# Optimization experiments

Measured on AMD Instinct MI355X. Metric: run time of the kernel, lower is better.

Reference implementation:

```python
import jax, jax.numpy as jnp
import numpy as np

# cfg dims: B batch, LQ max_que_len, O max_opt_count, LO max_opt_len,
# S max_sent_para, W max_words_sent, D word_emb
B, LQ, O, LO, S, W, D = 64, 64, 8, 32, 64, 32, 512
NEG_BIG = -9.0e15  # torch masked_fill constant for empty sentences


def setup_inputs() -> dict:
    key = jax.random.key(0)
    k1, k2, k3 = jax.random.split(key, 3)
    que_feat = jax.random.normal(k1, (B, LQ, D), dtype=jnp.float32)
    opt_feat = jax.random.normal(k2, (B, O, LO, D), dtype=jnp.float32)
    csf = jax.random.normal(k3, (B, S, W, D), dtype=jnp.float32)
    csf_mask = jnp.zeros((B, S, W), dtype=bool)   # True = padding word
    opt_sum = jnp.zeros((B, O), dtype=bool)       # True = empty option
    return dict(que_feat=que_feat, opt_feat=opt_feat, csf=csf,
                csf_mask=csf_mask, opt_sum=opt_sum)


def reference(que_feat, opt_feat, csf, csf_mask, opt_sum):
    b, s, w, d = csf.shape
    o = opt_feat.shape[1]

    # per-sentence valid length; empty sentences get a huge-magnitude divisor
    csf_len = jnp.sum(~csf_mask, axis=-1)                      # [B,S]
    csf_len = jnp.where(csf_len == 0, NEG_BIG,
                        csf_len.astype(jnp.float32))

    # question -> context sentence score: sum over query words and sentence
    # words of dot products (original: matmul + two sums, fused here)
    att_q2c = jnp.einsum('bqd,bswd->bs', que_feat, csf)        # [B,S]
    ix_q2c = jnp.argmax(att_q2c / csf_len, axis=-1)            # [B]

    # gather best sentence per batch item, broadcast over options
    que_csf = jnp.take_along_axis(
        csf, ix_q2c[:, None, None, None], axis=1)[:, 0]        # [B,W,D]
    que_csf = jnp.broadcast_to(que_csf[:, None], (b, o, w, d))
    que_csf = jnp.where(opt_sum[:, :, None, None], 0.0, que_csf)

    # option -> context sentence score
    att_o2c = jnp.einsum('bold,bswd->bos', opt_feat, csf)      # [B,O,S]
    ix_o2c = jnp.argmax(att_o2c / csf_len[:, None, :], axis=-1)  # [B,O]

    # faithful to original get_opt2csf: indexes csf[0] for EVERY batch item
    opt_csf = csf[0][ix_o2c]                                   # [B,O,W,D]
    opt_csf = jnp.where(opt_sum[:, :, None, None], 0.0, opt_csf)

    # make_mask: positions whose feature vector is all-zero
    que_csf_mask = jnp.sum(jnp.abs(que_csf), axis=-1) == 0     # [B,O,W]
    opt_csf_mask = jnp.sum(jnp.abs(opt_csf), axis=-1) == 0     # [B,O,W]
    return que_csf, que_csf_mask, opt_csf, opt_csf_mask
```

## Files before the change

kernel.cpp:

```cpp
#include <hip/hip_runtime.h>
#include <hip/hip_cooperative_groups.h>
#include <stddef.h>

namespace cg = cooperative_groups;

#define B  64
#define LQ 64
#define O  8
#define LO 32
#define S  64
#define W  32
#define D  512

#define NEG_BIG (-9.0e15f)

#define QUE_CSF_SZ  (B*O*W*D)
#define MASK_SZ     (B*O*W)
#define OFF_QMASK   (QUE_CSF_SZ)
#define OFF_OPT     (QUE_CSF_SZ + MASK_SZ)
#define OFF_OMASK   (QUE_CSF_SZ + MASK_SZ + QUE_CSF_SZ)

#define WS_QSUMH 0
#define WS_OSUM  (B*2*D)
#define WS_SC    (B*2*D + B*O*D)

#define NBLK 2368

using f4 = __attribute__((ext_vector_type(4))) float;

__device__ inline float dot4(f4 a, f4 b) {
  return a.x * b.x + a.y * b.y + a.z * b.z + a.w * b.w;
}

#define RED(v)                \
  do {                        \
    v += __shfl_xor(v, 32);   \
    v += __shfl_xor(v, 16);   \
    v += __shfl_xor(v, 8);    \
    v += __shfl_xor(v, 4);    \
    v += __shfl_xor(v, 2);    \
    v += __shfl_xor(v, 1);    \
  } while (0)

__device__ inline f4 stream32(const f4* __restrict__ p, int t) {
  f4 acc = {0.f, 0.f, 0.f, 0.f};
  #pragma unroll 8
  for (int r = 0; r < 32; ++r) acc += p[(size_t)r * 128 + t];
  return acc;
}

__device__ inline void dots9(const float* __restrict__ ws, f4 acc, int b,
                             int wv, int lane, float part[2][9]) {
  const f4* qh = (const f4*)(ws + WS_QSUMH) + (size_t)b * 256;
  const int t = wv * 64 + lane;
  f4 qs = qh[t] + qh[128 + t];
  float pq = dot4(acc, qs);
  float po[O];
  #pragma unroll
  for (int o = 0; o < O; ++o)
    po[o] = dot4(acc, ((const f4*)(ws + WS_OSUM))[((size_t)(b * O + o)) * 128 + t]);
  RED(pq);
  #pragma unroll
  for (int o = 0; o < O; ++o) RED(po[o]);
  if (lane == 0) {
    part[wv][0] = pq;
    #pragma unroll
    for (int o = 0; o < O; ++o) part[wv][1 + o] = po[o];
  }
}

__global__ __launch_bounds__(128, 5) void k_fused(
    const float* __restrict__ que, const float* __restrict__ opt,
    const float* __restrict__ csf, const unsigned char* __restrict__ csf_mask,
    float* __restrict__ ws) {
  const int blk = blockIdx.x;
  const int t = threadIdx.x;
  const int wv = t >> 6;
  const int lane = t & 63;
  const int g1 = blk + NBLK;
  const bool j1csf = (g1 < 4096);

  f4 acc0 = stream32((const f4*)csf + (size_t)blk * 4096, t);
  f4 acc1;
  if (j1csf) {
    acc1 = stream32((const f4*)csf + (size_t)g1 * 4096, t);
  } else if (g1 < 4224) {
    const int idx = g1 - 4096;
    const int b = idx >> 1, h = idx & 1;
    acc1 = stream32((const f4*)que + ((size_t)b * LQ + h * 32) * 128, t);
    ((f4*)(ws + WS_QSUMH))[(size_t)idx * 128 + t] = acc1;
  } else {
    const int bo = g1 - 4224;
    acc1 = stream32((const f4*)opt + (size_t)bo * LO * 128, t);
    ((f4*)(ws + WS_OSUM))[(size_t)bo * 128 + t] = acc1;
  }

  __threadfence();
  cg::this_grid().sync();

  __shared__ float part[2][2][9];
  dots9(ws, acc0, blk >> 6, wv, lane, part[0]);
  if (j1csf) dots9(ws, acc1, g1 >> 6, wv, lane, part[1]);

  float len;
  {
    const int bs = (wv == 0) ? blk : g1;
    int pad = 0;
    if (lane < W && (wv == 0 || j1csf))
      pad = (csf_mask[(size_t)bs * W + lane] != 0) ? 1 : 0;
    const unsigned long long bal = __ballot(pad);
    const int valid = W - (int)__popcll(bal);
    len = (valid == 0) ? NEG_BIG : (float)valid;
  }
  __syncthreads();

  if (t < 9) {
    const int b0 = blk >> 6, s0 = blk & 63;
    ws[WS_SC + ((size_t)t * B + b0) * S + s0] =
        (part[0][0][t] + part[0][1][t]) / len;
  }
  if (j1csf && t >= 64 && t < 73) {
    const int q = t - 64;
    const int b1 = g1 >> 6, s1 = g1 & 63;
    ws[WS_SC + ((size_t)q * B + b1) * S + s1] =
        (part[1][0][q] + part[1][1][q]) / len;
  }
}

template <int ROWS>
__device__ inline void rowsum4(const f4* __restrict__ src, f4* __restrict__ dst,
                               int t) {
  const int quarter = t >> 7;
  const int col = t & 127;
  const f4* p = src + (size_t)(quarter * (ROWS / 4)) * 128 + col;
  f4 acc = {0.f, 0.f, 0.f, 0.f};
  #pragma unroll
  for (int r = 0; r < ROWS / 4; ++r) acc += p[(size_t)r * 128];
  __shared__ f4 tmp[3][128];
  if (quarter) tmp[quarter - 1][col] = acc;
  __syncthreads();
  if (quarter == 0) dst[col] = acc + tmp[0][col] + tmp[1][col] + tmp[2][col];
}

__global__ __launch_bounds__(512) void k_qosum(
    const float* __restrict__ que, const float* __restrict__ opt,
    float* __restrict__ ws) {
  const int blk = blockIdx.x;
  const int t = threadIdx.x;
  if (blk < B) {
    rowsum4<LQ>((const f4*)que + (size_t)blk * LQ * 128,
                (f4*)(ws + WS_QSUMH) + (size_t)blk * 256, t);
    if (t < 128) {
      f4 z = {0.f, 0.f, 0.f, 0.f};
      ((f4*)(ws + WS_QSUMH))[(size_t)blk * 256 + 128 + t] = z;
    }
  } else {
    const int bo = blk - B;
    rowsum4<LO>((const f4*)opt + (size_t)bo * LO * 128,
                (f4*)(ws + WS_OSUM) + (size_t)bo * 128, t);
  }
}

__global__ __launch_bounds__(128) void k_score(
    const float* __restrict__ csf, const unsigned char* __restrict__ csf_mask,
    float* __restrict__ ws) {
  const int bs = blockIdx.x;
  const int b = bs >> 6;
  const int s = bs & 63;
  const int t = threadIdx.x;
  const int wv = t >> 6;
  const int lane = t & 63;

  f4 acc = stream32((const f4*)csf + (size_t)bs * 4096, t);

  __shared__ float part[2][9];
  dots9(ws, acc, b, wv, lane, part);

  int pad = 0;
  if (lane < W) pad = (csf_mask[(size_t)bs * W + lane] != 0) ? 1 : 0;
  const unsigned long long bal = __ballot(pad);
  const int valid = W - (int)__popcll(bal);
  const float len = (valid == 0) ? NEG_BIG : (float)valid;

  __syncthreads();
  if (t < 9)
    ws[WS_SC + ((size_t)t * B + b) * S + s] = (part[0][t] + part[1][t]) / len;
}

__global__ __launch_bounds__(128) void k_gather(
    const float* __restrict__ csf, const unsigned char* __restrict__ opt_sum,
    const float* __restrict__ ws, float* __restrict__ out) {
  const int bow = blockIdx.x;
  const int w = bow & 31;
  const int bo = bow >> 5;
  const int b = bo >> 3;
  const int o = bo & 7;
  const int t = threadIdx.x;
  const int wv = t >> 6;
  const int lane = t & 63;

  __shared__ int sh_ix[2];
  {
    const int q = (wv == 0) ? 0 : (1 + o);
    float v = ws[WS_SC + ((size_t)q * B + b) * S + lane];
    int idx = lane;
    for (int off = 32; off; off >>= 1) {
      float ov = __shfl_xor(v, off);
      int oi = __shfl_xor(idx, off);
      if (ov > v || (ov == v && oi < idx)) { v = ov; idx = oi; }
    }
    if (lane == 0) sh_ix[wv] = idx;
  }
  __syncthreads();

  const bool zero = (opt_sum[bo] != 0);
  f4 vq = {0.f, 0.f, 0.f, 0.f};
  f4 vo = {0.f, 0.f, 0.f, 0.f};
  if (!zero) {
    const int iq = sh_ix[0];
    const int io = sh_ix[1];
    vq = ((const f4*)csf)[(((size_t)b * S + iq) * W + w) * 128 + t];
    vo = ((const f4*)csf)[((size_t)io * W + w) * 128 + t];
  }
  __builtin_nontemporal_store(vq, (f4*)(out + (size_t)bow * D) + t);
  __builtin_nontemporal_store(vo, (f4*)(out + OFF_OPT + (size_t)bow * D) + t);

  float aq = fabsf(vq.x) + fabsf(vq.y) + fabsf(vq.z) + fabsf(vq.w);
  float ao = fabsf(vo.x) + fabsf(vo.y) + fabsf(vo.z) + fabsf(vo.w);
  for (int off = 32; off; off >>= 1) {
    aq += __shfl_xor(aq, off);
    ao += __shfl_xor(ao, off);
  }

  __shared__ float sq[2], so[2];
  if (lane == 0) { sq[wv] = aq; so[wv] = ao; }
  __syncthreads();
  if (t == 0) {
    out[OFF_QMASK + bow] = ((sq[0] + sq[1]) == 0.f) ? 1.f : 0.f;
    out[OFF_OMASK + bow] = ((so[0] + so[1]) == 0.f) ? 1.f : 0.f;
  }
}

extern "C" void kernel_launch(void* const* d_in, const int* in_sizes, int n_in,
                              void* d_out, int out_size, void* d_ws, size_t ws_size,
                              hipStream_t stream) {
  const float* que = (const float*)d_in[0];
  const float* opt = (const float*)d_in[1];
  const float* csf = (const float*)d_in[2];
  const unsigned char* csf_mask = (const unsigned char*)d_in[3];
  const unsigned char* opt_sum = (const unsigned char*)d_in[4];
  float* out = (float*)d_out;
  float* ws = (float*)d_ws;

  int coop = 0;
  {
    int dev = 0;
    hipDeviceProp_t prop{};
    int mb = 0;
    if (hipGetDevice(&dev) == hipSuccess &&
        hipGetDeviceProperties(&prop, dev) == hipSuccess &&
        hipOccupancyMaxActiveBlocksPerMultiprocessor(&mb, k_fused, 128, 0) ==
            hipSuccess) {
      if (prop.cooperativeLaunch &&
          (long)mb * prop.multiProcessorCount >= NBLK)
        coop = 1;
    }
  }

  if (coop) {
    void* args[] = {(void*)&que, (void*)&opt, (void*)&csf, (void*)&csf_mask,
                    (void*)&ws};
    if (hipLaunchCooperativeKernel(k_fused, dim3(NBLK), dim3(128), args, 0,
                                   stream) != hipSuccess)
      coop = 0;
  }
  if (!coop) {
    k_qosum<<<B + B * O, 512, 0, stream>>>(que, opt, ws);
    k_score<<<B * S, 128, 0, stream>>>(csf, csf_mask, ws);
  }

  k_gather<<<B * O * W, 128, 0, stream>>>(csf, opt_sum, ws, out);
}
```

Before: 70.63 us.

## Fuse gather phase into cooperative kernel behind a second grid sync

Moves the argmax plus gather/mask stage into the cooperative fused kernel after an extra grid barrier. Each wave handles one output row in a grid-stride loop, which removes the separate k_gather launch. The two streaming reductions are also interleaved in one loop so their loads can overlap. In exchange it adds a second grid-wide sync, and the gather runs at 128-thread occupancy with the argmax recomputed per row.

New measurement: 70.59 us. About the same (-0.1%).

```diff
diff --git a/kernel.cpp b/kernel.cpp
--- a/kernel.cpp
+++ b/kernel.cpp
@@ -42,12 +42,14 @@
     v += __shfl_xor(v, 1);    \
   } while (0)
 
-__device__ inline f4 stream32(const f4* __restrict__ p, int t) {
-  f4 acc = {0.f, 0.f, 0.f, 0.f};
-  #pragma unroll 8
-  for (int r = 0; r < 32; ++r) acc += p[(size_t)r * 128 + t];
-  return acc;
-}
+#define ARGMAX(v, idx)                                         \
+  do {                                                         \
+    for (int off_ = 32; off_; off_ >>= 1) {                    \
+      float ov_ = __shfl_xor(v, off_);                         \
+      int oi_ = __shfl_xor(idx, off_);                         \
+      if (ov_ > v || (ov_ == v && oi_ < idx)) { v = ov_; idx = oi_; } \
+    }                                                          \
+  } while (0)
 
 __device__ inline void dots9(const float* __restrict__ ws, f4 acc, int b,
                              int wv, int lane, float part[2][9]) {
@@ -72,7 +74,8 @@
 __global__ __launch_bounds__(128, 5) void k_fused(
     const float* __restrict__ que, const float* __restrict__ opt,
     const float* __restrict__ csf, const unsigned char* __restrict__ csf_mask,
-    float* __restrict__ ws) {
+    const unsigned char* __restrict__ opt_sum, float* __restrict__ ws,
+    float* __restrict__ out) {
   const int blk = blockIdx.x;
   const int t = threadIdx.x;
   const int wv = t >> 6;
@@ -80,19 +83,24 @@
   const int g1 = blk + NBLK;
   const bool j1csf = (g1 < 4096);
 
-  f4 acc0 = stream32((const f4*)csf + (size_t)blk * 4096, t);
-  f4 acc1;
-  if (j1csf) {
-    acc1 = stream32((const f4*)csf + (size_t)g1 * 4096, t);
-  } else if (g1 < 4224) {
-    const int idx = g1 - 4096;
-    const int b = idx >> 1, h = idx & 1;
-    acc1 = stream32((const f4*)que + ((size_t)b * LQ + h * 32) * 128, t);
-    ((f4*)(ws + WS_QSUMH))[(size_t)idx * 128 + t] = acc1;
-  } else {
-    const int bo = g1 - 4224;
-    acc1 = stream32((const f4*)opt + (size_t)bo * LO * 128, t);
-    ((f4*)(ws + WS_OSUM))[(size_t)bo * 128 + t] = acc1;
+  const f4* p0 = (const f4*)csf + (size_t)blk * 4096 + t;
+  const f4* p1;
+  if (j1csf)            p1 = (const f4*)csf + (size_t)g1 * 4096 + t;
+  else if (g1 < 4224)   p1 = (const f4*)que + (size_t)(g1 - 4096) * 4096 + t;
+  else                  p1 = (const f4*)opt + (size_t)(g1 - 4224) * 4096 + t;
+
+  f4 acc0 = {0.f, 0.f, 0.f, 0.f};
+  f4 acc1 = {0.f, 0.f, 0.f, 0.f};
+  #pragma unroll 8
+  for (int r = 0; r < 32; ++r) {
+    acc0 += p0[(size_t)r * 128];
+    acc1 += p1[(size_t)r * 128];
+  }
+  if (!j1csf) {
+    if (g1 < 4224)
+      ((f4*)(ws + WS_QSUMH))[(size_t)(g1 - 4096) * 128 + t] = acc1;
+    else
+      ((f4*)(ws + WS_OSUM))[(size_t)(g1 - 4224) * 128 + t] = acc1;
   }
 
   __threadfence();
@@ -124,6 +132,51 @@
     const int b1 = g1 >> 6, s1 = g1 & 63;
     ws[WS_SC + ((size_t)q * B + b1) * S + s1] =
         (part[1][0][q] + part[1][1][q]) / len;
+  }
+
+  __threadfence();
+  cg::this_grid().sync();
+
+  for (int row = blk * 2 + wv; row < B * O * W; row += NBLK * 2) {
+    const int w = row & 31;
+    const int bo = row >> 5;
+    const int b = bo >> 3;
+    const int o = bo & 7;
+
+    float vq_ = ws[WS_SC + (size_t)b * S + lane];
+    int iq = lane;
+    ARGMAX(vq_, iq);
+    float vo_ = ws[WS_SC + ((size_t)(1 + o) * B + b) * S + lane];
+    int io = lane;
+    ARGMAX(vo_, io);
+
+    const bool zero = (opt_sum[bo] != 0);
+    f4 a0 = {0.f, 0.f, 0.f, 0.f}, a1 = a0, b0 = a0, b1 = a0;
+    if (!zero) {
+      const f4* qrow = (const f4*)csf + (((size_t)b * S + iq) * W + w) * 128;
+      a0 = qrow[lane];
+      a1 = qrow[64 + lane];
+      const f4* orow = (const f4*)csf + ((size_t)io * W + w) * 128;
+      b0 = orow[lane];
+      b1 = orow[64 + lane];
+    }
+    f4* oq = (f4*)(out + (size_t)row * D);
+    f4* oo = (f4*)(out + OFF_OPT + (size_t)row * D);
+    __builtin_nontemporal_store(a0, oq + lane);
+    __builtin_nontemporal_store(a1, oq + 64 + lane);
+    __builtin_nontemporal_store(b0, oo + lane);
+    __builtin_nontemporal_store(b1, oo + 64 + lane);
+
+    float aq = fabsf(a0.x) + fabsf(a0.y) + fabsf(a0.z) + fabsf(a0.w) +
+               fabsf(a1.x) + fabsf(a1.y) + fabsf(a1.z) + fabsf(a1.w);
+    float ao = fabsf(b0.x) + fabsf(b0.y) + fabsf(b0.z) + fabsf(b0.w) +
+               fabsf(b1.x) + fabsf(b1.y) + fabsf(b1.z) + fabsf(b1.w);
+    RED(aq);
+    RED(ao);
+    if (lane == 0) {
+      out[OFF_QMASK + row] = (aq == 0.f) ? 1.f : 0.f;
+      out[OFF_OMASK + row] = (ao == 0.f) ? 1.f : 0.f;
+    }
   }
 }
 
@@ -171,7 +224,10 @@
   const int wv = t >> 6;
   const int lane = t & 63;
 
-  f4 acc = stream32((const f4*)csf + (size_t)bs * 4096, t);
+  const f4* p = (const f4*)csf + (size_t)bs * 4096 + t;
+  f4 acc = {0.f, 0.f, 0.f, 0.f};
+  #pragma unroll 8
+  for (int r = 0; r < 32; ++r) acc += p[(size_t)r * 128];
 
   __shared__ float part[2][9];
   dots9(ws, acc, b, wv, lane, part);
@@ -204,11 +260,7 @@
     const int q = (wv == 0) ? 0 : (1 + o);
     float v = ws[WS_SC + ((size_t)q * B + b) * S + lane];
     int idx = lane;
-    for (int off = 32; off; off >>= 1) {
-      float ov = __shfl_xor(v, off);
-      int oi = __shfl_xor(idx, off);
-      if (ov > v || (ov == v && oi < idx)) { v = ov; idx = oi; }
-    }
+    ARGMAX(v, idx);
     if (lane == 0) sh_ix[wv] = idx;
   }
   __syncthreads();
@@ -227,10 +279,8 @@
 
   float aq = fabsf(vq.x) + fabsf(vq.y) + fabsf(vq.z) + fabsf(vq.w);
   float ao = fabsf(vo.x) + fabsf(vo.y) + fabsf(vo.z) + fabsf(vo.w);
-  for (int off = 32; off; off >>= 1) {
-    aq += __shfl_xor(aq, off);
-    ao += __shfl_xor(ao, off);
-  }
+  RED(aq);
+  RED(ao);
 
   __shared__ float sq[2], so[2];
   if (lane == 0) { sq[wv] = aq; so[wv] = ao; }
@@ -269,7 +319,7 @@
 
   if (coop) {
     void* args[] = {(void*)&que, (void*)&opt, (void*)&csf, (void*)&csf_mask,
-                    (void*)&ws};
+                    (void*)&opt_sum, (void*)&ws, (void*)&out};
     if (hipLaunchCooperativeKernel(k_fused, dim3(NBLK), dim3(128), args, 0,
                                    stream) != hipSuccess)
       coop = 0;
@@ -277,7 +327,6 @@
   if (!coop) {
     k_qosum<<<B + B * O, 512, 0, stream>>>(que, opt, ws);
     k_score<<<B * S, 128, 0, stream>>>(csf, csf_mask, ws);
-  }
-
-  k_gather<<<B * O * W, 128, 0, stream>>>(csf, opt_sum, ws, out);
-}
+    k_gather<<<B * O * W, 128, 0, stream>>>(csf, opt_sum, ws, out);
+  }
+}
```
